# Kernel optimization log

Measured on AMD Instinct MI355X. Metric: run time of the kernel, lower is better.

Reference implementation:

```python
import jax, jax.numpy as jnp
import numpy as np

B, T, D = 2, 4096, 1024
H = 8
HD = D // H            # head_dim = 128
STRIDES = (1, 1, 2, 2, 4, 4, 8, 8)   # resolution_schedule
BANDS = 8              # spectral_bands
RH = 256               # router_hidden


def setup_inputs() -> dict:
    key = jax.random.key(0)
    ks = jax.random.split(key, 12)
    def xavier(k, shape):
        fan_in, fan_out = shape[-2], shape[-1]
        lim = 0.5 * (6.0 / (fan_in + fan_out)) ** 0.5   # gain=0.5 xavier_uniform
        return jax.random.uniform(k, shape, jnp.float32, -lim, lim)
    return {
        "x":          jax.random.normal(ks[0], (B, T, D), jnp.float32),
        "Wq":         xavier(ks[1], (H, D, HD)),
        "Wk":         xavier(ks[2], (H, D, HD)),
        "Wv":         xavier(ks[3], (H, D, HD)),
        "band_gates": jax.random.normal(ks[4], (H, BANDS), jnp.float32) * 0.1,
        "alphas":     jax.random.normal(ks[5], (H,), jnp.float32) * 0.1,
        "rW1":        xavier(ks[6], (D, RH)),
        "rb1":        jnp.zeros((RH,), jnp.float32),
        "rW2":        xavier(ks[7], (RH, H)),
        "rb2":        jnp.zeros((H,), jnp.float32),
        "Wout":       xavier(ks[8], (HD, D)),
    }


def _flux_head(x, Wq, Wk, Wv, band_gate, alpha, stride):
    # one FluxHead: strided K/V pooling + spectral logit gating + contra-flow residual
    q = jnp.einsum('btd,dh->bth', x, Wq)          # [B,T,HD]
    k = jnp.einsum('btd,dh->bth', x, Wk)
    v = jnp.einsum('btd,dh->bth', x, Wv)
    Tk = T // stride
    k = k.reshape(B, Tk, stride, HD).mean(axis=2)  # avg-pool K/V along time
    v = v.reshape(B, Tk, stride, HD).mean(axis=2)
    logits = jnp.einsum('bth,bkh->btk', q, k) / jnp.sqrt(jnp.float32(HD))  # [B,T,Tk]
    # spectral frequency gating on logits (rFFT over key axis, per-band sigmoid gain)
    F = jnp.fft.rfft(logits, axis=-1)              # [B,T,Tk//2+1] complex
    nbins = F.shape[-1]
    band_idx = jnp.clip((jnp.arange(nbins) * BANDS) // nbins, 0, BANDS - 1)
    gains = jax.nn.sigmoid(band_gate)[band_idx]    # [nbins]
    logits = jnp.fft.irfft(F * gains, n=Tk, axis=-1)
    attn = jax.nn.softmax(logits, axis=-1)
    out = jnp.einsum('btk,bkh->bth', attn, v)      # [B,T,HD]
    # contra-flow: reverse-sequence residual with learned gate
    return out + jnp.tanh(alpha) * out[:, ::-1, :]


def reference(x, Wq, Wk, Wv, band_gates, alphas, rW1, rb1, rW2, rb2, Wout):
    head_outs = [
        _flux_head(x, Wq[h], Wk[h], Wv[h], band_gates[h], alphas[h], STRIDES[h])
        for h in range(H)
    ]
    stacked = jnp.stack(head_outs, axis=2)                      # [B,T,H,HD]
    hid = jax.nn.relu(jnp.einsum('btd,dr->btr', x, rW1) + rb1)  # router MLP
    w = jax.nn.softmax(jnp.einsum('btr,rh->bth', hid, rW2) + rb2, axis=-1)
    mixed = jnp.einsum('bth,bthc->btc', w, stacked)             # [B,T,HD]
    return jnp.einsum('btc,cd->btd', mixed, Wout)               # [B,T,D]
```

## Files before the change

### kernel.cpp

```cpp
#include <hip/hip_runtime.h>
#include <hip/hip_bf16.h>

typedef __attribute__((ext_vector_type(8))) short short8;
typedef __attribute__((ext_vector_type(4))) short short4v;
typedef __attribute__((ext_vector_type(4))) float f32x4;
typedef unsigned short u16;

#define T_ 4096
#define D_ 1024
#define ISSL2E (0.08838834764831845f * 1.4426950408889634f)

__device__ __forceinline__ u16 f2bf(float f) {
  union { float f; unsigned u; } v; v.f = f;
  unsigned r = v.u + 0x7FFFu + ((v.u >> 16) & 1u);
  return (u16)(r >> 16);
}
__device__ __forceinline__ float bf2f(u16 u) {
  union { unsigned u; float f; } v; v.u = ((unsigned)u) << 16; return v.f;
}

__global__ __launch_bounds__(256) void prep_all(const float* __restrict__ x,
    const float* __restrict__ Wq, const float* __restrict__ Wk, const float* __restrict__ Wv,
    const float* __restrict__ rW1, const float* __restrict__ Wout, const float* __restrict__ bg,
    u16* __restrict__ p1, u16* __restrict__ p2, u16* __restrict__ p4, u16* __restrict__ p8,
    u16* __restrict__ wqT, u16* __restrict__ kvT, u16* __restrict__ rw1T, u16* __restrict__ woutT,
    u16* __restrict__ crep) {
  const int blk = blockIdx.x;
  const int tid = threadIdx.x;
  if (blk < 1024) {
    const int b = blk >> 9, t0 = (blk & 511) << 3;
    const float* src = x + ((long)b * T_ + t0) * D_;
#pragma unroll
    for (int j = 0; j < 4; ++j) {
      const int c = tid + j * 256;
      float v[8];
#pragma unroll
      for (int r = 0; r < 8; ++r) v[r] = src[r * D_ + c];
#pragma unroll
      for (int r = 0; r < 8; ++r) p1[((long)b * 4096 + t0 + r) * D_ + c] = f2bf(v[r]);
#pragma unroll
      for (int r = 0; r < 4; ++r)
        p2[((long)b * 2048 + (t0 >> 1) + r) * D_ + c] = f2bf((v[2*r] + v[2*r+1]) * 0.5f);
#pragma unroll
      for (int r = 0; r < 2; ++r)
        p4[((long)b * 1024 + (t0 >> 2) + r) * D_ + c] =
            f2bf((v[4*r] + v[4*r+1] + v[4*r+2] + v[4*r+3]) * 0.25f);
      p8[((long)b * 512 + (t0 >> 3)) * D_ + c] =
          f2bf((v[0]+v[1]+v[2]+v[3]+v[4]+v[5]+v[6]+v[7]) * 0.125f);
    }
    return;
  }
  if (blk < 14848) {
    const int idx = (blk - 1024) * 256 + tid;
    if (idx < 1048576) {
      const int h = idx >> 17, wi = idx & 131071;
      const int c = wi >> 10, k = wi & 1023;
      wqT[idx] = f2bf(Wq[(long)h * 131072 + k * 128 + c]);
    } else if (idx < 3145728) {
      const int lid = idx - 1048576;
      const int g = lid >> 19, wi = lid & 524287;
      const int n = wi >> 10, k = wi & 1023;
      const int kv = n >> 8, hh = (n >> 7) & 1, c = n & 127;
      const float* W = kv ? Wv : Wk;
      kvT[lid] = f2bf(W[(long)(2 * g + hh) * 131072 + k * 128 + c]);
    } else if (idx < 3407872) {
      const int lid = idx - 3145728;
      const int n = lid >> 10, k = lid & 1023;
      rw1T[lid] = f2bf(rW1[(long)k * 256 + n]);
    } else if (idx < 3538944) {
      const int lid = idx - 3407872;
      const int n = lid >> 7, k = lid & 127;
      woutT[lid] = f2bf(Wout[(long)k * 1024 + n]);
    }
    return;
  }
  const int rel = blk - 14848;
  const int h = rel >> 4, xi = rel & 15;
  const int Tk = 4096 >> (h >> 1);
  const int mask = Tk - 1;
  if (xi * 256 >= Tk) return;
  const int nb = (Tk >> 1) + 1;
  __shared__ float ct[4096];
  __shared__ float wm[2049];
  const float w0 = 6.283185307179586f / (float)Tk;
  for (int j = tid; j < Tk; j += 256) ct[j] = cosf(w0 * (float)j);
  for (int m = tid; m < nb; m += 256) {
    int band = (m * 8) / nb; if (band > 7) band = 7;
    const float g = 1.f / (1.f + expf(-bg[h * 8 + band]));
    const float sc = (m == 0 || m == nb - 1) ? 1.f : 2.f;
    wm[m] = g * sc / (float)Tk;
  }
  __syncthreads();
  const int n = xi * 256 + tid;
  float acc = 0.f;
  int idx = 0;
  for (int m = 0; m < nb; ++m) {
    acc += wm[m] * ct[idx];
    idx += n;
    if (idx >= Tk) idx -= Tk;
  }
  const u16 bf = f2bf(acc);
  u16* hb = crep + (long)h * 16416;
#pragma unroll
  for (int p = 0; p < 4; ++p) {
    const int q = (n - p) & mask;
    hb[p * 4104 + q] = bf;
    if (q < 8) hb[p * 4104 + q + Tk] = bf;
  }
}

__device__ __forceinline__ void gll16(const void* g, void* l) {
  __builtin_amdgcn_global_load_lds((const __attribute__((address_space(1))) void*)g,
                                   (__attribute__((address_space(3))) void*)l, 16, 0, 0);
}

__device__ __forceinline__ void gemm_core(const u16* __restrict__ A, const u16* __restrict__ Bt,
    void* __restrict__ Cv, int K, int lda, int ldb, int ldc, int tm, int tn, float alpha,
    int mode, u16 (*lds)[2][128][32],
    u16* KTp = nullptr, u16* VTp = nullptr, int Tkv = 0, int bsel = 0) {
  const int tid = threadIdx.x, lane = tid & 63, wid = tid >> 6;
  const int wr = wid >> 1, wc = wid & 1;
  const int srow = lane >> 2;
  const int scol = ((lane & 3) ^ ((lane >> 3) & 3)) * 8;
  const u16* ga0 = A + (long)(tm + 32 * wid + srow) * lda + scol;
  const u16* ga1 = ga0 + (long)16 * lda;
  const u16* gb0 = Bt + (long)(tn + 32 * wid + srow) * ldb + scol;
  const u16* gb1 = gb0 + (long)16 * ldb;
  f32x4 acc[4][4] = {};
  const int nk = K >> 5;
  gll16(ga0, &lds[0][0][32 * wid][0]);
  gll16(ga1, &lds[0][0][32 * wid + 16][0]);
  gll16(gb0, &lds[0][1][32 * wid][0]);
  gll16(gb1, &lds[0][1][32 * wid + 16][0]);
  int buf = 0;
  const int fr = lane & 15;
  const int fo2 = (((lane >> 4) & 3) ^ ((lane >> 1) & 3)) * 8;
  for (int kt = 0; kt < nk; ++kt) {
    __syncthreads();
    if (kt + 1 < nk) {
      const long ko = (long)(kt + 1) * 32;
      gll16(ga0 + ko, &lds[buf ^ 1][0][32 * wid][0]);
      gll16(ga1 + ko, &lds[buf ^ 1][0][32 * wid + 16][0]);
      gll16(gb0 + ko, &lds[buf ^ 1][1][32 * wid][0]);
      gll16(gb1 + ko, &lds[buf ^ 1][1][32 * wid + 16][0]);
    }
    short8 af[4], bfr[4];
#pragma unroll
    for (int i = 0; i < 4; ++i) {
      af[i]  = *(const short8*)&lds[buf][0][wr * 64 + i * 16 + fr][fo2];
      bfr[i] = *(const short8*)&lds[buf][1][wc * 64 + i * 16 + fr][fo2];
    }
#pragma unroll
    for (int i = 0; i < 4; ++i)
#pragma unroll
      for (int j = 0; j < 4; ++j)
        acc[i][j] = __builtin_amdgcn_mfma_f32_16x16x32_bf16(af[i], bfr[j], acc[i][j], 0, 0, 0);
    buf ^= 1;
  }
  const int er = (lane >> 4) * 4, ec = lane & 15;
  if (mode == 2) {
    const int tb = tm - bsel * Tkv + wr * 64;
#pragma unroll
    for (int i = 0; i < 4; ++i) {
      const int t0 = tb + i * 16 + er;
      const int kperm = (t0 & ~63) | (((t0 >> 4) & 1) << 5) | (((t0 >> 2) & 3) << 3)
                      | (((t0 >> 5) & 1) << 2);
#pragma unroll
      for (int j = 0; j < 4; ++j) {
        const int col = tn + wc * 64 + j * 16 + ec;
        const int kv = col >> 8, hh = (col >> 7) & 1, c = col & 127;
        u16* dstb = (kv ? VTp : KTp) + ((long)(hh * 2 + bsel) * 128 + c) * Tkv;
        short4v v;
#pragma unroll
        for (int r = 0; r < 4; ++r) v[r] = (short)f2bf(acc[i][j][r]);
        *(short4v*)(dstb + (kv ? kperm : t0)) = v;
      }
    }
  } else if (mode == 1) {
    u16* C = (u16*)Cv;
#pragma unroll
    for (int i = 0; i < 4; ++i)
#pragma unroll
      for (int j = 0; j < 4; ++j)
#pragma unroll
        for (int r = 0; r < 4; ++r)
          C[(long)(tm + wr * 64 + i * 16 + er + r) * ldc + (tn + wc * 64 + j * 16 + ec)] =
              f2bf(acc[i][j][r] * alpha);
  } else {
    float* C = (float*)Cv;
#pragma unroll
    for (int i = 0; i < 4; ++i)
#pragma unroll
      for (int j = 0; j < 4; ++j)
#pragma unroll
        for (int r = 0; r < 4; ++r)
          C[(long)(tm + wr * 64 + i * 16 + er + r) * ldc + (tn + wc * 64 + j * 16 + ec)] =
              acc[i][j][r] * alpha;
  }
}

template <bool OBF>
__global__ __launch_bounds__(256) void gemm_bt(const u16* __restrict__ A, const u16* __restrict__ Bt,
                                               void* __restrict__ Cv, int K, int lda, int ldb, int ldc,
                                               long abs_, long bbs, long cbs, float alpha) {
  __shared__ u16 lds[2][2][128][32];
  const u16* Az = A + (long)blockIdx.z * abs_;
  const u16* Bz = Bt + (long)blockIdx.z * bbs;
  void* Cz = OBF ? (void*)((u16*)Cv + (long)blockIdx.z * cbs)
                 : (void*)((float*)Cv + (long)blockIdx.z * cbs);
  gemm_core(Az, Bz, Cz, K, lda, ldb, ldc, blockIdx.x * 128, blockIdx.y * 128, alpha,
            OBF ? 1 : 0, lds);
}

__global__ __launch_bounds__(256) void gemm_p1(const u16* __restrict__ xbf,
    const u16* __restrict__ wqT, const u16* __restrict__ kvT, const u16* __restrict__ rw1T,
    u16* __restrict__ Qb, u16* __restrict__ KT, u16* __restrict__ VT, float* __restrict__ hid) {
  __shared__ u16 lds[2][2][128][32];
  const int bid = blockIdx.x;
  const int id = (bid & 7) * 140 + (bid >> 3);
  if (id < 512) {
    gemm_core(xbf, wqT, Qb, 1024, 1024, 1024, 1024,
              (id >> 3) * 128, (id & 7) * 128, 1.f, 1, lds);
  } else if (id < 992) {
    const int lid = id - 512;
    const int rt = lid >> 2, y = lid & 3;
    int g, lr;
    if (rt < 64)       { g = 0; lr = rt; }
    else if (rt < 96)  { g = 1; lr = rt - 64; }
    else if (rt < 112) { g = 2; lr = rt - 96; }
    else               { g = 3; lr = rt - 112; }
    const long xofs[4] = {0, 8388608, 12582912, 14680064};
    const long ktoff[4] = {0, 2097152, 3145728, 3670016};
    const int Tk = 4096 >> g;
    const int tm = lr * 128;
    const int bsel = (tm >= Tk) ? 1 : 0;
    gemm_core(xbf + xofs[g], kvT + (long)g * 524288, nullptr,
              1024, 1024, 1024, 0, tm, y * 128, 1.f, 2, lds,
              KT + ktoff[g], VT + ktoff[g], Tk, bsel);
  } else {
    const int lid = id - 992;
    gemm_core(xbf, rw1T, hid, 1024, 1024, 1024, 256,
              (lid >> 1) * 128, (lid & 1) * 128, 1.f, 0, lds);
  }
}

__global__ __launch_bounds__(256) void conv_k(const u16* __restrict__ crep,
    const u16* __restrict__ KT, u16* __restrict__ Kp) {
  const int bid = blockIdx.x;
  const int j = (bid & 7) * 30 + (bid >> 3);
  int z, lx;
  if (j < 128)      { z = j >> 5;             lx = j & 31; }
  else if (j < 192) { z = 4 + ((j - 128) >> 4); lx = (j - 128) & 15; }
  else if (j < 224) { z = 8 + ((j - 192) >> 3); lx = (j - 192) & 7; }
  else              { z = 12 + ((j - 224) >> 2); lx = (j - 224) & 3; }
  const int h = z >> 1, b = z & 1, g = h >> 1;
  const int Tk = 4096 >> g, mask = Tk - 1;
  const int tm = lx << 7;
  __shared__ u16 clds[16416];
  __shared__ u16 blds[2][4][128][32];
  const int tid = threadIdx.x, lane = tid & 63, wid = tid >> 6;
  const int wr = wid >> 1, wc = wid & 1;
  const int srow = lane >> 2;
  const int scol = ((lane & 3) ^ ((lane >> 3) & 3)) * 8;
  const int fr = lane & 15, fo = (lane >> 4) * 8;
  const int fo2 = (((lane >> 4) & 3) ^ ((lane >> 1) & 3)) * 8;
  {
    const short8* src = (const short8*)(crep + (long)h * 16416);
    short8* dst = (short8*)clds;
    for (int jj = tid; jj < 2052; jj += 256) dst[jj] = src[jj];
  }
  const long ktofs = 4194304 - (4194304 >> g);
  const u16* Bt = KT + ktofs + (long)((h & 1) * 2 + b) * 128 * Tk;
  u16* out = Kp + ktofs + ((long)(h & 1) << 8) * Tk + ((long)b << 7) * Tk;
  const u16* gb0 = Bt + (long)(32 * wid + srow) * Tk + scol;
  const u16* gb1 = gb0 + (long)16 * Tk;
  f32x4 acc[4][4] = {};
  int base[4];
#pragma unroll
  for (int i = 0; i < 4; ++i) base[i] = (fo - (tm + wr * 64 + i * 16 + fr)) & mask;
  const int p = base[0] & 3;
  const u16* crow = clds + p * 4104;
  const int nk = Tk >> 7;
#pragma unroll
  for (int c = 0; c < 4; ++c) {
    gll16(gb0 + c * 32, &blds[0][c][32 * wid][0]);
    gll16(gb1 + c * 32, &blds[0][c][32 * wid + 16][0]);
  }
  int buf = 0;
  for (int kt = 0; kt < nk; ++kt) {
    __syncthreads();
    if (kt + 1 < nk) {
      const long ko = (long)(kt + 1) * 128;
#pragma unroll
      for (int c = 0; c < 4; ++c) {
        gll16(gb0 + ko + c * 32, &blds[buf ^ 1][c][32 * wid][0]);
        gll16(gb1 + ko + c * 32, &blds[buf ^ 1][c][32 * wid + 16][0]);
      }
    }
#pragma unroll
    for (int c = 0; c < 4; ++c) {
      short8 af[4], bfr[4];
#pragma unroll
      for (int i = 0; i < 4; ++i) {
        const int a0 = base[i] ^ p;
        short4v lo = *(const short4v*)(crow + a0);
        short4v hi = *(const short4v*)(crow + a0 + 4);
        af[i][0] = lo[0]; af[i][1] = lo[1]; af[i][2] = lo[2]; af[i][3] = lo[3];
        af[i][4] = hi[0]; af[i][5] = hi[1]; af[i][6] = hi[2]; af[i][7] = hi[3];
        base[i] = (base[i] + 32) & mask;
        bfr[i] = *(const short8*)&blds[buf][c][wc * 64 + i * 16 + fr][fo2];
      }
#pragma unroll
      for (int i = 0; i < 4; ++i)
#pragma unroll
        for (int jj = 0; jj < 4; ++jj)
          acc[i][jj] = __builtin_amdgcn_mfma_f32_16x16x32_bf16(af[i], bfr[jj], acc[i][jj], 0, 0, 0);
    }
    buf ^= 1;
  }
  const int er = (lane >> 4) * 4, ec = lane & 15;
#pragma unroll
  for (int i = 0; i < 4; ++i)
#pragma unroll
    for (int jj = 0; jj < 4; ++jj)
#pragma unroll
      for (int r = 0; r < 4; ++r)
        out[(long)(tm + wr * 64 + i * 16 + er + r) * 128 + (wc * 64 + jj * 16 + ec)] =
            f2bf(acc[i][jj][r] * ISSL2E);
}

__global__ __launch_bounds__(256, 2) void flash(const u16* __restrict__ Qb,
    const u16* __restrict__ Kp, const u16* __restrict__ VT, u16* __restrict__ O) {
  const int wg = blockIdx.x;
  const int x = wg & 7, s = wg >> 3;
  const int t4 = s >> 4;
  const int lvl = t4 ^ (t4 >> 1);
  const int hh = x >> 2, b = (x >> 1) & 1;
  const int h = lvl * 2 + hh;
  const int qtm = (((x & 1) << 4) + (s & 15)) << 7;
  const int Tk = 4096 >> lvl;
  const int nt = Tk >> 6;

  __shared__ __align__(16) char smem[65536];
  u16 (*Kl)[4][64][32] = (u16(*)[4][64][32])smem;
  u16 (*Vl)[128][64]   = (u16(*)[128][64])(smem + 32768);

  const int tid = threadIdx.x, lane = tid & 63, wid = tid >> 6;
  const int fr = lane & 15, gs = lane >> 4;
  const int fo = gs * 8;
  const int fo2 = ((gs & 3) ^ ((lane >> 1) & 3)) * 8;

  const long ktofs = 4194304 - (4194304 >> lvl);
  const u16* kbase = Kp + ktofs + (long)(hh * 2 + b) * 128 * Tk;
  const u16* vbase = VT + ktofs + (long)(hh * 2 + b) * 128 * Tk;

  short8 aq[2][4];
#pragma unroll
  for (int m = 0; m < 2; ++m)
#pragma unroll
    for (int kk = 0; kk < 4; ++kk)
      aq[m][kk] = *(const short8*)(Qb +
          ((long)(b * 4096 + qtm + wid * 32 + m * 16 + fr)) * 1024 + h * 128 + kk * 32 + fo);

  const u16* kptr = kbase + (long)(lane >> 2) * 128 + wid * 32 +
                    (((lane & 3) ^ ((lane >> 3) & 3)) << 3);
  const u16* vptr = vbase + (long)(32 * wid + (lane >> 3)) * Tk +
                    (((lane & 7) ^ ((lane >> 3) & 7)) << 3);

  const char* kbL  = smem + fr * 64 + fo2 * 2;
  const char* vbL0 = smem + 32768 + fr * 128 + ((((gs    ) ^ (fr & 7)) & 7) << 4);
  const char* vbL1 = smem + 32768 + fr * 128 + ((((gs ^ 4) ^ (fr & 7)) & 7) << 4);

  f32x4 acc[2][8] = {};
  f32x4 accl[2] = {};
  float mr[2] = {-3e38f, -3e38f};

  short8 ones;
#pragma unroll
  for (int i = 0; i < 8; ++i) ones[i] = (short)0x3F80;

#pragma unroll
  for (int i = 0; i < 4; ++i) {
    gll16(kptr + i * 2048, &Kl[0][wid][i * 16][0]);
    gll16(vptr + (long)i * 8 * Tk, &Vl[0][32 * wid + 8 * i][0]);
  }

  int cur = 0;
  for (int kt = 0; kt < nt; ++kt) {
    asm volatile("s_waitcnt vmcnt(0)" ::: "memory");
    __builtin_amdgcn_sched_barrier(0);
    __builtin_amdgcn_s_barrier();
    __builtin_amdgcn_sched_barrier(0);
    if (kt + 1 < nt) {
      const int ktn = kt + 1;
#pragma unroll
      for (int i = 0; i < 4; ++i) {
        gll16(kptr + (long)ktn * 8192 + i * 2048, &Kl[cur ^ 1][wid][i * 16][0]);
        gll16(vptr + (long)ktn * 64 + (long)i * 8 * Tk, &Vl[cur ^ 1][32 * wid + 8 * i][0]);
      }
    }
    const char* kc = kbL + cur * 16384;
    f32x4 sa[2][4] = {};
    __builtin_amdgcn_s_setprio(1);
#pragma unroll
    for (int kk = 0; kk < 4; ++kk) {
      short8 bk[4];
#pragma unroll
      for (int jm = 0; jm < 4; ++jm)
        bk[jm] = *(const short8*)(kc + kk * 4096 + jm * 1024);
#pragma unroll
      for (int m = 0; m < 2; ++m)
#pragma unroll
        for (int jm = 0; jm < 4; ++jm)
          sa[m][jm] = __builtin_amdgcn_mfma_f32_16x16x32_bf16(bk[jm], aq[m][kk], sa[m][jm], 0, 0, 0);
    }
    __builtin_amdgcn_s_setprio(0);
    float tmx[2];
#pragma unroll
    for (int m = 0; m < 2; ++m) {
      float v0 = fmaxf(fmaxf(sa[m][0][0], sa[m][0][1]), fmaxf(sa[m][0][2], sa[m][0][3]));
      float v1 = fmaxf(fmaxf(sa[m][1][0], sa[m][1][1]), fmaxf(sa[m][1][2], sa[m][1][3]));
      float v2 = fmaxf(fmaxf(sa[m][2][0], sa[m][2][1]), fmaxf(sa[m][2][2], sa[m][2][3]));
      float v3 = fmaxf(fmaxf(sa[m][3][0], sa[m][3][1]), fmaxf(sa[m][3][2], sa[m][3][3]));
      float v = fmaxf(fmaxf(v0, v1), fmaxf(v2, v3));
      v = fmaxf(v, __shfl_xor(v, 16));
      v = fmaxf(v, __shfl_xor(v, 32));
      tmx[m] = v;
    }
    const bool need = (tmx[0] > mr[0] + 8.f) | (tmx[1] > mr[1] + 8.f);
    if (__any((int)need)) {
#pragma unroll
      for (int m = 0; m < 2; ++m) {
        const float mn = fmaxf(mr[m], tmx[m]);
        const float av = __builtin_amdgcn_exp2f(mr[m] - mn);
        mr[m] = mn;
#pragma unroll
        for (int jd = 0; jd < 8; ++jd)
#pragma unroll
          for (int r = 0; r < 4; ++r) acc[m][jd][r] *= av;
#pragma unroll
        for (int r = 0; r < 4; ++r) accl[m][r] *= av;
      }
    }
#pragma unroll
    for (int m = 0; m < 2; ++m)
#pragma unroll
      for (int jm = 0; jm < 4; ++jm)
#pragma unroll
        for (int r = 0; r < 4; ++r)
          sa[m][jm][r] = __builtin_amdgcn_exp2f(sa[m][jm][r] - mr[m]);
    unsigned pk[2][4][2];
#pragma unroll
    for (int m = 0; m < 2; ++m)
#pragma unroll
      for (int jm = 0; jm < 4; ++jm) {
        asm("v_cvt_pk_bf16_f32 %0, %1, %2" : "=v"(pk[m][jm][0]) : "v"(sa[m][jm][0]), "v"(sa[m][jm][1]));
        asm("v_cvt_pk_bf16_f32 %0, %1, %2" : "=v"(pk[m][jm][1]) : "v"(sa[m][jm][2]), "v"(sa[m][jm][3]));
      }
    const char* vc0 = vbL0 + cur * 16384;
    const char* vc1 = vbL1 + cur * 16384;
    __builtin_amdgcn_s_setprio(1);
#pragma unroll
    for (int kk = 0; kk < 2; ++kk) {
      short8 pt[2];
#pragma unroll
      for (int m = 0; m < 2; ++m) {
        union { unsigned u[4]; short8 s; } pp;
        pp.u[0] = pk[m][kk][0];     pp.u[1] = pk[m][kk][1];
        pp.u[2] = pk[m][kk + 2][0]; pp.u[3] = pk[m][kk + 2][1];
        pt[m] = pp.s;
      }
      const char* vc = kk ? vc1 : vc0;
#pragma unroll
      for (int jd = 0; jd < 8; ++jd) {
        short8 bb = *(const short8*)(vc + jd * 2048);
#pragma unroll
        for (int m = 0; m < 2; ++m)
          acc[m][jd] = __builtin_amdgcn_mfma_f32_16x16x32_bf16(bb, pt[m], acc[m][jd], 0, 0, 0);
      }
#pragma unroll
      for (int m = 0; m < 2; ++m)
        accl[m] = __builtin_amdgcn_mfma_f32_16x16x32_bf16(ones, pt[m], accl[m], 0, 0, 0);
    }
    __builtin_amdgcn_s_setprio(0);
    cur ^= 1;
  }
  __syncthreads();
  float* Ot = (float*)smem;
  float* ot = Ot + wid * 16 * 132;
#pragma unroll
  for (int m = 0; m < 2; ++m) {
    const float inv = 1.f / accl[m][0];
#pragma unroll
    for (int jd = 0; jd < 8; ++jd) {
      f32x4 v;
#pragma unroll
      for (int r = 0; r < 4; ++r) v[r] = acc[m][jd][r] * inv;
      *(f32x4*)&ot[fr * 132 + jd * 16 + gs * 4] = v;
    }
    asm volatile("s_waitcnt lgkmcnt(0)" ::: "memory");
    __builtin_amdgcn_sched_barrier(0);
    const int q = qtm + wid * 32 + m * 16 + (lane >> 2);
    u16* od = O + ((long)(b * 4096 + q) * 8 + h) * 128 + (lane & 3) * 32;
#pragma unroll
    for (int j = 0; j < 8; ++j) {
      f32x4 v = *(const f32x4*)&ot[(lane >> 2) * 132 + (lane & 3) * 32 + j * 4];
      short4v s;
#pragma unroll
      for (int r = 0; r < 4; ++r) s[r] = (short)f2bf(v[r]);
      *(short4v*)(od + j * 4) = s;
    }
    asm volatile("s_waitcnt lgkmcnt(0)" ::: "memory");
    __builtin_amdgcn_sched_barrier(0);
  }
}

__global__ __launch_bounds__(256) void router_mix(const float* __restrict__ hid,
    const float* __restrict__ rb1, const float* __restrict__ rW2, const float* __restrict__ rb2,
    const float* __restrict__ al, const u16* __restrict__ O, u16* __restrict__ mixed) {
  const int tok = blockIdx.x;
  const int b = tok >> 12, t = tok & 4095;
  const int tid = threadIdx.x;
  __shared__ float lred[4][8];
  __shared__ float wgt[8];
  __shared__ float ta[8];
  const float hv = fmaxf(hid[(long)tok * 256 + tid] + rb1[tid], 0.f);
  const float4* w4 = (const float4*)(rW2 + tid * 8);
  const float4 wa = w4[0], wb = w4[1];
  float part[8] = {hv * wa.x, hv * wa.y, hv * wa.z, hv * wa.w,
                   hv * wb.x, hv * wb.y, hv * wb.z, hv * wb.w};
#pragma unroll
  for (int h = 0; h < 8; ++h) {
    float v = part[h];
#pragma unroll
    for (int o = 1; o < 64; o <<= 1) v += __shfl_xor(v, o);
    if ((tid & 63) == 0) lred[tid >> 6][h] = v;
  }
  __syncthreads();
  if (tid < 8) ta[tid] = tanhf(al[tid]);
  if (tid == 0) {
    float lg[8], m = -1e30f;
#pragma unroll
    for (int h = 0; h < 8; ++h) {
      lg[h] = lred[0][h] + lred[1][h] + lred[2][h] + lred[3][h] + rb2[h];
      m = fmaxf(m, lg[h]);
    }
    float s = 0.f;
#pragma unroll
    for (int h = 0; h < 8; ++h) { lg[h] = __expf(lg[h] - m); s += lg[h]; }
    const float inv = 1.f / s;
#pragma unroll
    for (int h = 0; h < 8; ++h) wgt[h] = lg[h] * inv;
  }
  __syncthreads();
  if (tid < 128) {
    const long base = (long)tok * 1024 + tid;
    const long rbase = ((long)b * 4096 + (4095 - t)) * 1024 + tid;
    float acc = 0.f;
#pragma unroll
    for (int h = 0; h < 8; ++h)
      acc += wgt[h] * (bf2f(O[base + h * 128]) + ta[h] * bf2f(O[rbase + h * 128]));
    mixed[(long)tok * 128 + tid] = f2bf(acc);
  }
}

extern "C" void kernel_launch(void* const* d_in, const int* in_sizes, int n_in,
                              void* d_out, int out_size, void* d_ws, size_t ws_size,
                              hipStream_t stream) {
  const float* x    = (const float*)d_in[0];
  const float* Wq   = (const float*)d_in[1];
  const float* Wk   = (const float*)d_in[2];
  const float* Wv   = (const float*)d_in[3];
  const float* bg   = (const float*)d_in[4];
  const float* al   = (const float*)d_in[5];
  const float* rW1  = (const float*)d_in[6];
  const float* rb1  = (const float*)d_in[7];
  const float* rW2  = (const float*)d_in[8];
  const float* rb2  = (const float*)d_in[9];
  const float* Wout = (const float*)d_in[10];
  float* out = (float*)d_out;

  const size_t MB = 1u << 20;
  char* w = (char*)d_ws;
  u16*   xbf   = (u16*)(w + 0);
  u16*   O     = (u16*)(w + 0);
  u16*   Qb    = (u16*)(w + 32 * MB);
  u16*   Kp    = (u16*)(w + 48 * MB);
  u16*   KT    = (u16*)(w + 63 * MB);
  u16*   VT    = (u16*)(w + 70 * MB + 512 * 1024);
  float* hid   = (float*)(w + 78 * MB);
  u16*   wqT   = (u16*)(w + 86 * MB);
  u16*   kvT   = (u16*)(w + 88 * MB);
  u16*   rw1T  = (u16*)(w + 92 * MB);
  u16*   woutT = (u16*)(w + 92 * MB + 512 * 1024);
  u16*   crep  = (u16*)(w + 92 * MB + 768 * 1024);
  u16*   mixed = (u16*)(w + 93 * MB + 512 * 1024);
  u16*   xp2   = (u16*)(w + 16 * MB);
  u16*   xp4   = (u16*)(w + 24 * MB);
  u16*   xp8   = (u16*)(w + 28 * MB);

  prep_all<<<dim3(14976), dim3(256), 0, stream>>>(x, Wq, Wk, Wv, rW1, Wout, bg,
      xbf, xp2, xp4, xp8, wqT, kvT, rw1T, woutT, crep);

  gemm_p1<<<dim3(1120), dim3(256), 0, stream>>>(xbf, wqT, kvT, rw1T, Qb, KT, VT, hid);

  conv_k<<<dim3(240), dim3(256), 0, stream>>>(crep, KT, Kp);

  flash<<<dim3(512), dim3(256), 0, stream>>>(Qb, Kp, VT, O);

  router_mix<<<dim3(8192), dim3(256), 0, stream>>>(hid, rb1, rW2, rb2, al, O, mixed);
  gemm_bt<false><<<dim3(64, 8), dim3(256), 0, stream>>>(mixed, woutT, out,
      128, 128, 128, 1024, 0, 0, 0, 1.f);
}
```

Baseline: 312.2 us.

## Split flash attention over key halves and merge partials in router kernel

The flash kernel now splits each query tile's key range into two halves, so the grid doubles to 1024 workgroups. Each half writes an unnormalized bf16 partial output plus its per-row max and sum to a new buffer. The router_mix kernel combines the two partials with log-sum-exp rescaling before mixing heads. The aim is better occupancy and load balance across CUs, since stride-1 heads dominate runtime. The cost is twice the O traffic and extra reads in router_mix, and storing the unnormalized partials in bf16 may lose some precision.

New measurement: 297.7 us. 1.05x faster.

```diff
diff --git a/kernel.cpp b/kernel.cpp
--- a/kernel.cpp
+++ b/kernel.cpp
@@ -330,16 +330,17 @@
 }
 
 __global__ __launch_bounds__(256, 2) void flash(const u16* __restrict__ Qb,
-    const u16* __restrict__ Kp, const u16* __restrict__ VT, u16* __restrict__ O) {
+    const u16* __restrict__ Kp, const u16* __restrict__ VT,
+    u16* __restrict__ Op, float* __restrict__ mlb) {
   const int wg = blockIdx.x;
   const int x = wg & 7, s = wg >> 3;
-  const int t4 = s >> 4;
-  const int lvl = t4 ^ (t4 >> 1);
-  const int hh = x >> 2, b = (x >> 1) & 1;
+  const int q4 = s >> 5;
+  const int lvl = q4 ^ (q4 >> 1);
+  const int hh = x >> 2, b = (x >> 1) & 1, kh = x & 1;
   const int h = lvl * 2 + hh;
-  const int qtm = (((x & 1) << 4) + (s & 15)) << 7;
+  const int qtm = (s & 31) << 7;
   const int Tk = 4096 >> lvl;
-  const int nt = Tk >> 6;
+  const int nt = Tk >> 7;
 
   __shared__ __align__(16) char smem[65536];
   u16 (*Kl)[4][64][32] = (u16(*)[4][64][32])smem;
@@ -351,7 +352,7 @@
   const int fo2 = ((gs & 3) ^ ((lane >> 1) & 3)) * 8;
 
   const long ktofs = 4194304 - (4194304 >> lvl);
-  const u16* kbase = Kp + ktofs + (long)(hh * 2 + b) * 128 * Tk;
+  const u16* kbase = Kp + ktofs + (long)(hh * 2 + b) * 128 * Tk + (long)kh * (Tk >> 1) * 128;
   const u16* vbase = VT + ktofs + (long)(hh * 2 + b) * 128 * Tk;
 
   short8 aq[2][4];
@@ -364,7 +365,7 @@
 
   const u16* kptr = kbase + (long)(lane >> 2) * 128 + wid * 32 +
                     (((lane & 3) ^ ((lane >> 3) & 3)) << 3);
-  const u16* vptr = vbase + (long)(32 * wid + (lane >> 3)) * Tk +
+  const u16* vptr = vbase + (long)(32 * wid + (lane >> 3)) * Tk + kh * (Tk >> 1) +
                     (((lane & 7) ^ ((lane >> 3) & 7)) << 3);
 
   const char* kbL  = smem + fr * 64 + fo2 * 2;
@@ -488,42 +489,46 @@
   __syncthreads();
   float* Ot = (float*)smem;
   float* ot = Ot + wid * 16 * 132;
+  u16* Obase = Op + (long)kh * 8388608;
 #pragma unroll
   for (int m = 0; m < 2; ++m) {
-    const float inv = 1.f / accl[m][0];
-#pragma unroll
-    for (int jd = 0; jd < 8; ++jd) {
-      f32x4 v;
-#pragma unroll
-      for (int r = 0; r < 4; ++r) v[r] = acc[m][jd][r] * inv;
-      *(f32x4*)&ot[fr * 132 + jd * 16 + gs * 4] = v;
-    }
+#pragma unroll
+    for (int jd = 0; jd < 8; ++jd)
+      *(f32x4*)&ot[fr * 132 + jd * 16 + gs * 4] = acc[m][jd];
     asm volatile("s_waitcnt lgkmcnt(0)" ::: "memory");
     __builtin_amdgcn_sched_barrier(0);
     const int q = qtm + wid * 32 + m * 16 + (lane >> 2);
-    u16* od = O + ((long)(b * 4096 + q) * 8 + h) * 128 + (lane & 3) * 32;
+    u16* od = Obase + ((long)(b * 4096 + q) * 8 + h) * 128 + (lane & 3) * 32;
 #pragma unroll
     for (int j = 0; j < 8; ++j) {
       f32x4 v = *(const f32x4*)&ot[(lane >> 2) * 132 + (lane & 3) * 32 + j * 4];
-      short4v s;
-#pragma unroll
-      for (int r = 0; r < 4; ++r) s[r] = (short)f2bf(v[r]);
-      *(short4v*)(od + j * 4) = s;
+      short4v sv;
+#pragma unroll
+      for (int r = 0; r < 4; ++r) sv[r] = (short)f2bf(v[r]);
+      *(short4v*)(od + j * 4) = sv;
     }
     asm volatile("s_waitcnt lgkmcnt(0)" ::: "memory");
     __builtin_amdgcn_sched_barrier(0);
+    if (gs == 0) {
+      const int q2 = qtm + wid * 32 + m * 16 + fr;
+      ((float2*)mlb)[(long)kh * 65536 + (long)(b * 4096 + q2) * 8 + h] =
+          make_float2(mr[m], accl[m][0]);
+    }
   }
 }
 
 __global__ __launch_bounds__(256) void router_mix(const float* __restrict__ hid,
     const float* __restrict__ rb1, const float* __restrict__ rW2, const float* __restrict__ rb2,
-    const float* __restrict__ al, const u16* __restrict__ O, u16* __restrict__ mixed) {
+    const float* __restrict__ al, const u16* __restrict__ Op, const float* __restrict__ mlb,
+    u16* __restrict__ mixed) {
   const int tok = blockIdx.x;
   const int b = tok >> 12, t = tok & 4095;
+  const int rtok = b * 4096 + (4095 - t);
   const int tid = threadIdx.x;
   __shared__ float lred[4][8];
   __shared__ float wgt[8];
   __shared__ float ta[8];
+  __shared__ float el[2][8][2];
   const float hv = fmaxf(hid[(long)tok * 256 + tid] + rb1[tid], 0.f);
   const float4* w4 = (const float4*)(rW2 + tid * 8);
   const float4 wa = w4[0], wb = w4[1];
@@ -536,6 +541,18 @@
     for (int o = 1; o < 64; o <<= 1) v += __shfl_xor(v, o);
     if ((tid & 63) == 0) lred[tid >> 6][h] = v;
   }
+  if (tid >= 64 && tid < 80) {
+    const int j = tid - 64;
+    const int h = j & 7, which = j >> 3;
+    const long tk = which ? rtok : tok;
+    const float2 a = ((const float2*)mlb)[tk * 8 + h];
+    const float2 c = ((const float2*)mlb)[65536 + tk * 8 + h];
+    const float M = fmaxf(a.x, c.x);
+    const float w1 = exp2f(a.x - M), w2 = exp2f(c.x - M);
+    const float inv = 1.f / (w1 * a.y + w2 * c.y);
+    el[which][h][0] = w1 * inv;
+    el[which][h][1] = w2 * inv;
+  }
   __syncthreads();
   if (tid < 8) ta[tid] = tanhf(al[tid]);
   if (tid == 0) {
@@ -555,11 +572,16 @@
   __syncthreads();
   if (tid < 128) {
     const long base = (long)tok * 1024 + tid;
-    const long rbase = ((long)b * 4096 + (4095 - t)) * 1024 + tid;
+    const long rbase = (long)rtok * 1024 + tid;
     float acc = 0.f;
 #pragma unroll
-    for (int h = 0; h < 8; ++h)
-      acc += wgt[h] * (bf2f(O[base + h * 128]) + ta[h] * bf2f(O[rbase + h * 128]));
+    for (int h = 0; h < 8; ++h) {
+      const float o = el[0][h][0] * bf2f(Op[base + h * 128]) +
+                      el[0][h][1] * bf2f(Op[8388608 + base + h * 128]);
+      const float orv = el[1][h][0] * bf2f(Op[rbase + h * 128]) +
+                        el[1][h][1] * bf2f(Op[8388608 + rbase + h * 128]);
+      acc += wgt[h] * (o + ta[h] * orv);
+    }
     mixed[(long)tok * 128 + tid] = f2bf(acc);
   }
 }
@@ -583,7 +605,7 @@
   const size_t MB = 1u << 20;
   char* w = (char*)d_ws;
   u16*   xbf   = (u16*)(w + 0);
-  u16*   O     = (u16*)(w + 0);
+  u16*   Op    = (u16*)(w + 0);
   u16*   Qb    = (u16*)(w + 32 * MB);
   u16*   Kp    = (u16*)(w + 48 * MB);
   u16*   KT    = (u16*)(w + 63 * MB);
@@ -595,6 +617,7 @@
   u16*   woutT = (u16*)(w + 92 * MB + 512 * 1024);
   u16*   crep  = (u16*)(w + 92 * MB + 768 * 1024);
   u16*   mixed = (u16*)(w + 93 * MB + 512 * 1024);
+  float* mlbuf = (float*)(w + 95 * MB + 512 * 1024);
   u16*   xp2   = (u16*)(w + 16 * MB);
   u16*   xp4   = (u16*)(w + 24 * MB);
   u16*   xp8   = (u16*)(w + 28 * MB);
@@ -606,9 +629,9 @@
 
   conv_k<<<dim3(240), dim3(256), 0, stream>>>(crep, KT, Kp);
 
-  flash<<<dim3(512), dim3(256), 0, stream>>>(Qb, Kp, VT, O);
-
-  router_mix<<<dim3(8192), dim3(256), 0, stream>>>(hid, rb1, rW2, rb2, al, O, mixed);
+  flash<<<dim3(1024), dim3(256), 0, stream>>>(Qb, Kp, VT, Op, mlbuf);
+
+  router_mix<<<dim3(8192), dim3(256), 0, stream>>>(hid, rb1, rW2, rb2, al, Op, mlbuf, mixed);
   gemm_bt<false><<<dim3(64, 8), dim3(256), 0, stream>>>(mixed, woutT, out,
       128, 128, 128, 1024, 0, 0, 0, 1.f);
 }
```
